# Kernel optimization log

Hardware: AMD Instinct MI355X
Metric: run time of the kernel (lower is better)

The kernel has to match this reference:

```python
import jax, jax.numpy as jnp
import numpy as np
from jax import lax

B, C, H, W = 32, 684, 16, 64
HID, A, CK, K = 256, 512, 512, 11


def setup_inputs() -> dict:
    key = jax.random.key(0)
    ks = jax.random.split(key, 12)
    s = 0.02
    return {
        "cnn_features": jax.random.normal(ks[0], (B, C, H, W), jnp.float32),
        "hidden": jax.random.normal(ks[1], (B, HID), jnp.float32),
        "alpha_sum": jax.random.uniform(ks[2], (B, 1, H, W), jnp.float32),
        "image_mask": jnp.ones((B, 1, H, W), jnp.float32),
        # hidden_weight: Linear(HID -> A)
        "Wh": jax.random.normal(ks[3], (A, HID), jnp.float32) * s,
        "bh": jnp.zeros((A,), jnp.float32),
        # encoder_feature_conv: Conv2d(C -> A, 1x1) == pointwise linear
        "Wec": jax.random.normal(ks[4], (A, C), jnp.float32) * s,
        "bec": jnp.zeros((A,), jnp.float32),
        # attention_conv: Conv2d(1 -> CK, 11x11, pad 5, no bias)
        "Wac": jax.random.normal(ks[5], (CK, 1, K, K), jnp.float32) * s,
        # attention_weight: Linear(CK -> A, no bias)
        "Waw": jax.random.normal(ks[6], (A, CK), jnp.float32) * s,
        # alpha_convert: Linear(A -> 1)
        "Wv": jax.random.normal(ks[7], (1, A), jnp.float32) * s,
        "bv": jnp.zeros((1,), jnp.float32),
    }


def reference(cnn_features, hidden, alpha_sum, image_mask,
              Wh, bh, Wec, bec, Wac, Waw, Wv, bv):
    # query = hidden_weight(hidden): [B, A]
    query = hidden @ Wh.T + bh
    # attention_conv(alpha_sum): [B, CK, H, W]
    ast = lax.conv_general_dilated(
        alpha_sum, Wac, window_strides=(1, 1),
        padding=[(K // 2, K // 2), (K // 2, K // 2)],
        dimension_numbers=("NCHW", "OIHW", "NCHW"))
    # attention_weight on permuted conv output: [B, H, W, A]
    coverage_alpha = jnp.einsum("bkhw,ak->bhwa", ast, Waw)
    # encoder_feature_conv (1x1 conv == pointwise linear): [B, H, W, A]
    cnn_trans = jnp.einsum("bchw,ac->bhwa", cnn_features, Wec) + bec
    # additive attention score
    alpha_score = jnp.tanh(query[:, None, None, :] + coverage_alpha + cnn_trans)
    # alpha_convert -> scalar energy per position: [B, H, W]
    energy = jnp.einsum("bhwa,a->bhw", alpha_score, Wv[0]) + bv[0]
    energy = energy - energy.max()  # global max-subtract as in original
    energy_exp = jnp.exp(energy) * image_mask[:, 0]
    denom = energy_exp.sum(axis=(-1, -2))[:, None, None] + 1e-10
    alpha = energy_exp / denom  # [B, H, W]
    alpha_sum_new = alpha[:, None, :, :] + alpha_sum  # [B, 1, H, W]
    # context: weighted spatial sum over features -> [B, C]
    context_vector = jnp.einsum("bhw,bchw->bc", alpha, cnn_features)
    return (context_vector, alpha, alpha_sum_new)
```

## Files before the change

kernel.cpp:

```cpp
#include <hip/hip_runtime.h>
#include <hip/hip_bf16.h>
#include <math.h>

#define Bn   32
#define Cn   684
#define Hn   16
#define Wn   64
#define HWn  1024
#define HIDn 256
#define An   512
#define KKn  121
#define CREAL 805
#define CPAD 832
#define NSTEP 26

#define OUT_ALPHA 21888
#define OUT_ASUM  (21888 + 32768)

typedef short short8 __attribute__((ext_vector_type(8)));
typedef float floatx4 __attribute__((ext_vector_type(4)));

__device__ __forceinline__ unsigned short f2bf(float f) {
    union { float f; unsigned int i; } v; v.f = f;
    unsigned int i = v.i;
    return (unsigned short)((i + 0x7fffu + ((i >> 16) & 1u)) >> 16);
}
__device__ __forceinline__ unsigned int cvt2(float lo, float hi) {
    __hip_bfloat162 h = __float22bfloat162_rn(float2{lo, hi});
    union { __hip_bfloat162 h; unsigned int u; } cv; cv.h = h;
    return cv.u;
}

__device__ __forceinline__ size_t bfr_idx(int n, int k) {
    return ((((size_t)(n >> 4) * 26 + (k >> 5)) * 64
             + ((k >> 3) & 3) * 16 + (n & 15)) * 8) + (k & 7);
}

__global__ __launch_bounds__(256) void k_prep(
    const float* __restrict__ hidden,
    const float* __restrict__ Wh,
    const float* __restrict__ bh,
    const float* __restrict__ bec,
    const float* __restrict__ Wec,
    const float* __restrict__ Wac,
    const float* __restrict__ Waw,
    float* __restrict__ query,
    unsigned short* __restrict__ Bfr,
    float* __restrict__ denom)
{
    __shared__ float sbuf[512];
    const int blk = blockIdx.x, t = threadIdx.x;
    if (blk < 512) {
        const int a = blk;
        sbuf[t]       = Waw[(size_t)a * 512 + t];
        sbuf[t + 256] = Waw[(size_t)a * 512 + t + 256];
        __syncthreads();
        for (int cp = t; cp < Cn; cp += 256)
            Bfr[bfr_idx(a, cp)] = f2bf(Wec[(size_t)a * Cn + cp]);
        if (t < KKn) {
            float s = 0.f;
            #pragma unroll 8
            for (int k = 0; k < 512; ++k)
                s = fmaf(sbuf[k], Wac[k * KKn + t], s);
            Bfr[bfr_idx(a, Cn + t)] = f2bf(s);
        }
        for (int cp = CREAL + t; cp < CPAD; cp += 256)
            Bfr[bfr_idx(a, cp)] = 0;
    } else if (blk < 544) {
        const int b = blk - 512;
        sbuf[t] = (t < HIDn) ? hidden[b * HIDn + t] : 0.f;
        __syncthreads();
        for (int a = t; a < An; a += 256) {
            const float4* wp = (const float4*)(Wh + (size_t)a * HIDn);
            float s = bh[a] + bec[a];
            #pragma unroll 8
            for (int i = 0; i < HIDn / 4; ++i) {
                float4 w = wp[i];
                s = fmaf(sbuf[4 * i],     w.x, s);
                s = fmaf(sbuf[4 * i + 1], w.y, s);
                s = fmaf(sbuf[4 * i + 2], w.z, s);
                s = fmaf(sbuf[4 * i + 3], w.w, s);
            }
            query[b * An + a] = s;
        }
    } else {
        if (t == 0) denom[blk - 544] = 1e-10f;
    }
}

__device__ __forceinline__ float fetchU(const float* __restrict__ Xb,
                                        const float* plane, const int* lut,
                                        int m, int row) {
    if (row < Cn) return Xb[(size_t)row * HWn + m];
    return plane[lut[row - Cn] + m];
}

__global__ __launch_bounds__(512, 4) void k_energy(
    const float* __restrict__ X,
    const float* __restrict__ asum,
    const float* __restrict__ Wv,
    const float* __restrict__ query,
    const unsigned short* __restrict__ Bfr,
    const float* __restrict__ mask,
    float* __restrict__ energy,
    float* __restrict__ denom)
{
    __shared__ __align__(16) unsigned short As[2][64 * 40];
    __shared__ float plane[878];
    __shared__ int   lut[148];
    __shared__ float qs[512];
    __shared__ float wvs[512];
    __shared__ float red[8][64];

    const int t = threadIdx.x;
    const int d = blockIdx.x;
    const int hh = d & 15, b = d >> 4;
    const int w = t >> 6, lane = t & 63;
    const int q = lane >> 4, r = lane & 15;
    const int mA = lane;

    const float* Xb = X + (size_t)b * Cn * HWn + hh * Wn;
    const unsigned short* Bp = Bfr + (size_t)(w * 4) * 26 * 512;

    for (int i = t; i < 878; i += 512) {
        float v = 0.f;
        if (i < 814) {
            int di = i / 74, cc = i - di * 74;
            int h2 = hh + di - 5, w2 = cc - 5;
            if (h2 >= 0 && h2 < Hn && w2 >= 0 && w2 < Wn)
                v = asum[b * HWn + h2 * Wn + w2];
        }
        plane[i] = v;
    }
    if (t < 148) {
        int off = 814;
        if (t < 121) { int di = t / 11; off = di * 74 + (t - di * 11); }
        lut[t] = off;
    }
    qs[t]  = query[b * An + t];
    wvs[t] = Wv[t];
    {
        const float* xp = Xb + (size_t)(w * 4) * HWn + mA;
        float v0 = xp[0];
        float v1 = xp[(size_t)1 * HWn];
        float v2 = xp[(size_t)2 * HWn];
        float v3 = xp[(size_t)3 * HWn];
        *(uint2*)&As[0][mA * 40 + w * 4] = make_uint2(cvt2(v0, v1), cvt2(v2, v3));
    }

    short8 bf[4], af[4];
    float va[4];

    {
        const float* xp = Xb + (size_t)(32 + w * 4) * HWn + mA;
        va[0] = xp[0];
        va[1] = xp[(size_t)1 * HWn];
        va[2] = xp[(size_t)2 * HWn];
        va[3] = xp[(size_t)3 * HWn];
    }
    #pragma unroll
    for (int nf = 0; nf < 4; ++nf)
        bf[nf] = *(const short8*)(Bp + ((size_t)(nf * 26)) * 512 + lane * 8);
    __syncthreads();

    floatx4 acc[4][4];
    #pragma unroll
    for (int mf = 0; mf < 4; ++mf)
        #pragma unroll
        for (int nf = 0; nf < 4; ++nf)
            acc[mf][nf] = (floatx4){0.f, 0.f, 0.f, 0.f};

#define READA(CUR) {                                                          \
    _Pragma("unroll")                                                         \
    for (int mf = 0; mf < 4; ++mf)                                            \
        af[mf] = *(const short8*)&As[CUR][(mf * 16 + r) * 40 + q * 8];        \
    }

#define WRITEA(CUR) {                                                         \
    *(uint2*)&As[CUR][mA * 40 + w * 4] =                                      \
        make_uint2(cvt2(va[0], va[1]), cvt2(va[2], va[3]));                   \
    }

#define MFMA16() {                                                            \
    __builtin_amdgcn_s_setprio(1);                                            \
    _Pragma("unroll")                                                         \
    for (int mf = 0; mf < 4; ++mf)                                            \
        _Pragma("unroll")                                                     \
        for (int nf = 0; nf < 4; ++nf)                                        \
            acc[mf][nf] = __builtin_amdgcn_mfma_f32_16x16x32_bf16(            \
                af[mf], bf[nf], acc[mf][nf], 0, 0, 0);                        \
    __builtin_amdgcn_s_setprio(0);                                            \
    }

#define ISSUE_BF(CC) {                                                        \
    _Pragma("unroll")                                                         \
    for (int nf = 0; nf < 4; ++nf)                                            \
        bf[nf] = *(const short8*)(Bp + ((size_t)(nf * 26 + (CC))) * 512       \
                                     + lane * 8);                             \
    }

#define LOOP_BARRIER() {                                                      \
    asm volatile("s_waitcnt lgkmcnt(0)" ::: "memory");                        \
    __builtin_amdgcn_sched_barrier(0);                                        \
    __builtin_amdgcn_s_barrier();                                             \
    __builtin_amdgcn_sched_barrier(0);                                        \
    }

    const float* xva = Xb + (size_t)(64 + w * 4) * HWn + mA;
    const size_t chstep = (size_t)32 * HWn;

    for (int ch = 0; ch < 18; ++ch) {
        const int cur = ch & 1;
        READA(cur);
        WRITEA(cur ^ 1);
        MFMA16();
        va[0] = xva[0];
        va[1] = xva[(size_t)1 * HWn];
        va[2] = xva[(size_t)2 * HWn];
        va[3] = xva[(size_t)3 * HWn];
        xva += chstep;
        ISSUE_BF(ch + 1);
        LOOP_BARRIER();
    }

    for (int ch = 18; ch < NSTEP; ++ch) {
        const int cur = ch & 1;
        READA(cur);
        if (ch < NSTEP - 1) WRITEA(cur ^ 1);
        MFMA16();
        const int cva = (ch + 2 <= 25) ? (ch + 2) : 25;
        const int c0 = cva * 32 + w * 4;
        #pragma unroll
        for (int j = 0; j < 4; ++j)
            va[j] = fetchU(Xb, plane, lut, mA, c0 + j);
        const int cbf = (ch + 1 <= 25) ? (ch + 1) : 25;
        ISSUE_BF(cbf);
        LOOP_BARRIER();
    }

#undef READA
#undef WRITEA
#undef MFMA16
#undef ISSUE_BF
#undef LOOP_BARRIER

    #pragma unroll
    for (int mf = 0; mf < 4; ++mf) {
        float ep4[4];
        #pragma unroll
        for (int rg = 0; rg < 4; ++rg) ep4[rg] = 0.f;
        #pragma unroll
        for (int nf = 0; nf < 4; ++nf) {
            int nl = w * 64 + nf * 16 + r;
            float qv = qs[nl], wv = wvs[nl];
            #pragma unroll
            for (int rg = 0; rg < 4; ++rg) {
                float x = acc[mf][nf][rg] + qv;
                float e2 = __expf(2.f * x);
                float th = 1.f - 2.f * __builtin_amdgcn_rcpf(e2 + 1.f);
                ep4[rg] = fmaf(wv, th, ep4[rg]);
            }
        }
        #pragma unroll
        for (int rg = 0; rg < 4; ++rg) {
            #pragma unroll
            for (int msk = 1; msk <= 8; msk <<= 1)
                ep4[rg] += __shfl_xor(ep4[rg], msk, 64);
        }
        if (r == 0) {
            #pragma unroll
            for (int rg = 0; rg < 4; ++rg)
                red[w][mf * 16 + q * 4 + rg] = ep4[rg];
        }
    }
    __syncthreads();
    if (t < 64) {
        float s = 0.f;
        #pragma unroll
        for (int ww = 0; ww < 8; ++ww) s += red[ww][t];
        float em = __expf(s) * mask[b * HWn + hh * Wn + t];
        energy[b * HWn + hh * Wn + t] = em;
        float ds = em;
        #pragma unroll
        for (int off = 32; off >= 1; off >>= 1)
            ds += __shfl_down(ds, off, 64);
        if (t == 0) atomicAdd(&denom[b], ds);
    }
}

__global__ __launch_bounds__(256) void k_ctx(
    const float* __restrict__ X,
    const float* __restrict__ expmask,
    const float* __restrict__ denom,
    const float* __restrict__ asum,
    float* __restrict__ out)
{
    __shared__ float al[1024];
    const int bx = blockIdx.x, b = blockIdx.y;
    const int t = threadIdx.x, lane = t & 63, wid = t >> 6;

    const float rd = 1.f / denom[b];
    #pragma unroll
    for (int i = 0; i < 4; ++i)
        al[i * 256 + t] = expmask[b * HWn + i * 256 + t] * rd;
    __syncthreads();

    const int c0 = bx * 16 + wid * 4;
    const float* xpc[4];
    #pragma unroll
    for (int cc = 0; cc < 4; ++cc) {
        int c = c0 + cc; if (c >= Cn) c = Cn - 1;
        xpc[cc] = X + ((size_t)(b * Cn + c)) * HWn;
    }
    float s0 = 0.f, s1 = 0.f, s2 = 0.f, s3 = 0.f;
    #pragma unroll
    for (int i = 0; i < 4; ++i) {
        const int off = i * 256 + lane * 4;
        float4 a = *(const float4*)(al + off);
        float4 x0 = *(const float4*)(xpc[0] + off);
        float4 x1 = *(const float4*)(xpc[1] + off);
        float4 x2 = *(const float4*)(xpc[2] + off);
        float4 x3 = *(const float4*)(xpc[3] + off);
        s0 = fmaf(a.x, x0.x, s0); s0 = fmaf(a.y, x0.y, s0);
        s0 = fmaf(a.z, x0.z, s0); s0 = fmaf(a.w, x0.w, s0);
        s1 = fmaf(a.x, x1.x, s1); s1 = fmaf(a.y, x1.y, s1);
        s1 = fmaf(a.z, x1.z, s1); s1 = fmaf(a.w, x1.w, s1);
        s2 = fmaf(a.x, x2.x, s2); s2 = fmaf(a.y, x2.y, s2);
        s2 = fmaf(a.z, x2.z, s2); s2 = fmaf(a.w, x2.w, s2);
        s3 = fmaf(a.x, x3.x, s3); s3 = fmaf(a.y, x3.y, s3);
        s3 = fmaf(a.z, x3.z, s3); s3 = fmaf(a.w, x3.w, s3);
    }
    float sv[4] = {s0, s1, s2, s3};
    #pragma unroll
    for (int cc = 0; cc < 4; ++cc) {
        float s = sv[cc];
        #pragma unroll
        for (int off = 32; off >= 1; off >>= 1)
            s += __shfl_down(s, off, 64);
        if (lane == 0 && c0 + cc < Cn) out[b * Cn + c0 + cc] = s;
    }

    if (bx == 0) {
        #pragma unroll
        for (int i = 0; i < 4; ++i) {
            int p = i * 256 + t;
            float a = al[p];
            out[OUT_ALPHA + b * HWn + p] = a;
            out[OUT_ASUM  + b * HWn + p] = a + asum[b * HWn + p];
        }
    }
}

extern "C" void kernel_launch(void* const* d_in, const int* in_sizes, int n_in,
                              void* d_out, int out_size, void* d_ws, size_t ws_size,
                              hipStream_t stream)
{
    const float* X      = (const float*)d_in[0];
    const float* hidden = (const float*)d_in[1];
    const float* asum   = (const float*)d_in[2];
    const float* mask   = (const float*)d_in[3];
    const float* Wh     = (const float*)d_in[4];
    const float* bh     = (const float*)d_in[5];
    const float* Wec    = (const float*)d_in[6];
    const float* bec    = (const float*)d_in[7];
    const float* Wac    = (const float*)d_in[8];
    const float* Waw    = (const float*)d_in[9];
    const float* Wv     = (const float*)d_in[10];
    (void)in_sizes; (void)n_in; (void)out_size; (void)ws_size;

    float* out = (float*)d_out;
    float* ws = (float*)d_ws;
    float* query  = ws;
    float* energy = ws + 16384;
    float* denom  = ws + 16384 + 32768;
    unsigned short* Bfr = (unsigned short*)(ws + 16384 + 32768 + 64);

    k_prep   <<<dim3(576),      dim3(256), 0, stream>>>(hidden, Wh, bh, bec,
                                                        Wec, Wac, Waw, query, Bfr, denom);
    k_energy <<<dim3(512),      dim3(512), 0, stream>>>(X, asum, Wv, query, Bfr,
                                                        mask, energy, denom);
    k_ctx    <<<dim3(43, 32),   dim3(256), 0, stream>>>(X, energy, denom, asum, out);
}
```

Measured before the change: 225.9 us.

## Process two K-chunks per barrier in energy GEMM and remap blocks per XCD

```diff
diff --git a/kernel.cpp b/kernel.cpp
--- a/kernel.cpp
+++ b/kernel.cpp
@@ -97,15 +97,15 @@
 
 __global__ __launch_bounds__(512, 4) void k_energy(
     const float* __restrict__ X,
-    const float* __restrict__ asum,
     const float* __restrict__ Wv,
     const float* __restrict__ query,
     const unsigned short* __restrict__ Bfr,
     const float* __restrict__ mask,
+    const float* __restrict__ asum,
     float* __restrict__ energy,
     float* __restrict__ denom)
 {
-    __shared__ __align__(16) unsigned short As[2][64 * 40];
+    __shared__ __align__(16) unsigned short As[4][64 * 42];
     __shared__ float plane[878];
     __shared__ int   lut[148];
     __shared__ float qs[512];
@@ -114,7 +114,8 @@
 
     const int t = threadIdx.x;
     const int d = blockIdx.x;
-    const int hh = d & 15, b = d >> 4;
+    const int xcd = d & 7, idx = d >> 3;
+    const int b = xcd * 4 + (idx >> 4), hh = idx & 15;
     const int w = t >> 6, lane = t & 63;
     const int q = lane >> 4, r = lane & 15;
     const int mA = lane;
@@ -139,24 +140,23 @@
     }
     qs[t]  = query[b * An + t];
     wvs[t] = Wv[t];
+
+    short8 bf[4], af[4];
+    float va[8];
+
     {
-        const float* xp = Xb + (size_t)(w * 4) * HWn + mA;
-        float v0 = xp[0];
-        float v1 = xp[(size_t)1 * HWn];
-        float v2 = xp[(size_t)2 * HWn];
-        float v3 = xp[(size_t)3 * HWn];
-        *(uint2*)&As[0][mA * 40 + w * 4] = make_uint2(cvt2(v0, v1), cvt2(v2, v3));
-    }
-
-    short8 bf[4], af[4];
-    float va[4];
-
+        const float* xp = Xb + (size_t)(w * 8) * HWn + mA;
+        #pragma unroll
+        for (int j = 0; j < 8; ++j) va[j] = xp[(size_t)j * HWn];
+        uint4 u;
+        u.x = cvt2(va[0], va[1]); u.y = cvt2(va[2], va[3]);
+        u.z = cvt2(va[4], va[5]); u.w = cvt2(va[6], va[7]);
+        *(uint4*)&As[w >> 2][mA * 42 + ((w * 8) & 31)] = u;
+    }
     {
-        const float* xp = Xb + (size_t)(32 + w * 4) * HWn + mA;
-        va[0] = xp[0];
-        va[1] = xp[(size_t)1 * HWn];
-        va[2] = xp[(size_t)2 * HWn];
-        va[3] = xp[(size_t)3 * HWn];
+        const float* xp = Xb + (size_t)(64 + w * 8) * HWn + mA;
+        #pragma unroll
+        for (int j = 0; j < 8; ++j) va[j] = xp[(size_t)j * HWn];
     }
     #pragma unroll
     for (int nf = 0; nf < 4; ++nf)
@@ -170,15 +170,17 @@
         for (int nf = 0; nf < 4; ++nf)
             acc[mf][nf] = (floatx4){0.f, 0.f, 0.f, 0.f};
 
-#define READA(CUR) {                                                          \
+#define READA(BUF) {                                                          \
     _Pragma("unroll")                                                         \
     for (int mf = 0; mf < 4; ++mf)                                            \
-        af[mf] = *(const short8*)&As[CUR][(mf * 16 + r) * 40 + q * 8];        \
-    }
-
-#define WRITEA(CUR) {                                                         \
-    *(uint2*)&As[CUR][mA * 40 + w * 4] =                                      \
-        make_uint2(cvt2(va[0], va[1]), cvt2(va[2], va[3]));                   \
+        af[mf] = *(const short8*)&As[BUF][(mf * 16 + r) * 42 + q * 8];        \
+    }
+
+#define WRITEA2(WB) {                                                         \
+    uint4 u;                                                                  \
+    u.x = cvt2(va[0], va[1]); u.y = cvt2(va[2], va[3]);                       \
+    u.z = cvt2(va[4], va[5]); u.w = cvt2(va[6], va[7]);                       \
+    *(uint4*)&As[(WB) + (w >> 2)][mA * 42 + ((w * 8) & 31)] = u;              \
     }
 
 #define MFMA16() {                                                            \
@@ -199,6 +201,18 @@
                                      + lane * 8);                             \
     }
 
+#define ISSUE_VA(S) {                                                         \
+    const int base = (2 * (S) + 4) * 32 + w * 8;                              \
+    if ((S) <= 7) {                                                           \
+        const float* xp = Xb + (size_t)base * HWn + mA;                       \
+        _Pragma("unroll")                                                     \
+        for (int j = 0; j < 8; ++j) va[j] = xp[(size_t)j * HWn];              \
+    } else {                                                                  \
+        _Pragma("unroll")                                                     \
+        for (int j = 0; j < 8; ++j)                                           \
+            va[j] = fetchU(Xb, plane, lut, mA, base + j);                     \
+    } }
+
 #define LOOP_BARRIER() {                                                      \
     asm volatile("s_waitcnt lgkmcnt(0)" ::: "memory");                        \
     __builtin_amdgcn_sched_barrier(0);                                        \
@@ -206,42 +220,24 @@
     __builtin_amdgcn_sched_barrier(0);                                        \
     }
 
-    const float* xva = Xb + (size_t)(64 + w * 4) * HWn + mA;
-    const size_t chstep = (size_t)32 * HWn;
-
-    for (int ch = 0; ch < 18; ++ch) {
-        const int cur = ch & 1;
-        READA(cur);
-        WRITEA(cur ^ 1);
+    for (int s = 0; s < 13; ++s) {
+        const int rb = (s & 1) << 1;
+        READA(rb);
+        if (s < 12) WRITEA2(rb ^ 2);
         MFMA16();
-        va[0] = xva[0];
-        va[1] = xva[(size_t)1 * HWn];
-        va[2] = xva[(size_t)2 * HWn];
-        va[3] = xva[(size_t)3 * HWn];
-        xva += chstep;
-        ISSUE_BF(ch + 1);
+        ISSUE_BF(2 * s + 1);
+        if (s < 11) ISSUE_VA(s);
+        READA(rb + 1);
+        MFMA16();
+        if (s < 12) ISSUE_BF(2 * s + 2);
         LOOP_BARRIER();
     }
 
-    for (int ch = 18; ch < NSTEP; ++ch) {
-        const int cur = ch & 1;
-        READA(cur);
-        if (ch < NSTEP - 1) WRITEA(cur ^ 1);
-        MFMA16();
-        const int cva = (ch + 2 <= 25) ? (ch + 2) : 25;
-        const int c0 = cva * 32 + w * 4;
-        #pragma unroll
-        for (int j = 0; j < 4; ++j)
-            va[j] = fetchU(Xb, plane, lut, mA, c0 + j);
-        const int cbf = (ch + 1 <= 25) ? (ch + 1) : 25;
-        ISSUE_BF(cbf);
-        LOOP_BARRIER();
-    }
-
 #undef READA
-#undef WRITEA
+#undef WRITEA2
 #undef MFMA16
 #undef ISSUE_BF
+#undef ISSUE_VA
 #undef LOOP_BARRIER
 
     #pragma unroll
@@ -377,7 +373,7 @@
 
     k_prep   <<<dim3(576),      dim3(256), 0, stream>>>(hidden, Wh, bh, bec,
                                                         Wec, Wac, Waw, query, Bfr, denom);
-    k_energy <<<dim3(512),      dim3(512), 0, stream>>>(X, asum, Wv, query, Bfr,
-                                                        mask, energy, denom);
+    k_energy <<<dim3(512),      dim3(512), 0, stream>>>(X, Wv, query, Bfr,
+                                                        mask, asum, energy, denom);
     k_ctx    <<<dim3(43, 32),   dim3(256), 0, stream>>>(X, energy, denom, asum, out);
 }
```

New measurement: 221.3 us. -2.1%, faster.
